# Optimization experiments

Hardware: AMD Instinct MI355X
Metric: run time of the kernel (lower is better)

## Reference

```python
import jax, jax.numpy as jnp
import numpy as np

B, S, H = 2, 2048, 2048
NH, NKV, HD = 16, 4, 128
THETA = 1000000.0

def _rope_tables(seq_len, dim, theta):
    inv_freq = 1.0 / (theta ** (np.arange(0, dim, 2, dtype=np.float32) / dim))
    t = np.arange(seq_len, dtype=np.float32)
    freqs = np.outer(t, inv_freq)                      # [S, dim/2]
    emb = np.concatenate([freqs, freqs], axis=-1)      # [S, dim]
    return jnp.asarray(np.cos(emb)), jnp.asarray(np.sin(emb))

def setup_inputs() -> dict:
    key = jax.random.key(0)
    ks = jax.random.split(key, 5)
    cos, sin = _rope_tables(S, HD, THETA)
    scale = 1.0 / np.sqrt(H)
    return {
        "x": jax.random.normal(ks[0], (B, S, H), jnp.float32),
        "cos": cos, "sin": sin,
        "wq": jax.random.normal(ks[1], (H, NH * HD), jnp.float32) * scale,
        "wk": jax.random.normal(ks[2], (H, NKV * HD), jnp.float32) * scale,
        "wv": jax.random.normal(ks[3], (H, NKV * HD), jnp.float32) * scale,
        "wo": jax.random.normal(ks[4], (NH * HD, H), jnp.float32) * scale,
    }

def _rotate_half(t):
    h = t.shape[-1] // 2
    return jnp.concatenate([-t[..., h:], t[..., :h]], axis=-1)

def reference(x, cos, sin, wq, wk, wv, wo):
    b, s, _ = x.shape
    n_rep = NH // NKV
    q = (x @ wq).reshape(b, s, NH, HD)    # [b,s,nh,hd]
    k = (x @ wk).reshape(b, s, NKV, HD)
    v = (x @ wv).reshape(b, s, NKV, HD)
    # RoPE: cos/sin [s,hd] broadcast over batch and heads
    c = cos[None, :, None, :]
    sn = sin[None, :, None, :]
    q = q * c + _rotate_half(q) * sn
    k = k * c + _rotate_half(k) * sn
    # GQA: repeat kv heads n_rep times
    k = jnp.repeat(k, n_rep, axis=2)      # [b,s,nh,hd]
    v = jnp.repeat(v, n_rep, axis=2)
    q = q.transpose(0, 2, 1, 3)           # [b,nh,s,hd]
    k = k.transpose(0, 2, 1, 3)
    v = v.transpose(0, 2, 1, 3)
    scores = jnp.einsum('bhqd,bhkd->bhqk', q, k) / jnp.sqrt(jnp.float32(HD))
    causal = jnp.tril(jnp.ones((s, s), dtype=bool))
    scores = jnp.where(causal[None, None], scores, jnp.float32(-jnp.inf))
    attn = jax.nn.softmax(scores.astype(jnp.float32), axis=-1).astype(q.dtype)
    out = jnp.einsum('bhqk,bhkd->bhqd', attn, v)
    out = out.transpose(0, 2, 1, 3).reshape(b, s, NH * HD)
    return out @ wo
```

## Files before the change

### kernel.cpp

```cpp
#include <hip/hip_runtime.h>
#include <hip/hip_bf16.h>

#define Bb 2
#define Ss 2048
#define Hh 2048
#define NH 16
#define NKV 4
#define HD 128
#define NREP (NH / NKV)
#define Mrows (Bb * Ss)
#define NQKV (NH*HD + 2*NKV*HD)

using short8 = __attribute__((ext_vector_type(8))) short;
using f32x4  = __attribute__((ext_vector_type(4))) float;

__device__ __forceinline__ unsigned short f2b(float f) {
  union { float f; unsigned u; } v; v.f = f;
  return (unsigned short)((v.u + 0x7fffu + ((v.u >> 16) & 1u)) >> 16);
}

__device__ __forceinline__ void gload16(const void* g, void* l) {
  __builtin_amdgcn_global_load_lds(
      (const __attribute__((address_space(1))) unsigned int*)g,
      (__attribute__((address_space(3))) unsigned int*)l, 16, 0, 0);
}

__global__ void prep(const float* __restrict__ x, unsigned short* __restrict__ xb,
                     const float* __restrict__ wq, const float* __restrict__ wk,
                     const float* __restrict__ wv, unsigned short* __restrict__ wqkvt,
                     const float* __restrict__ wo, unsigned short* __restrict__ wot) {
  __shared__ float tile[32][33];
  const int bid = blockIdx.x;
  const int t = threadIdx.x;
  if (bid < 8192) {
    int i = (bid * 256 + t) * 4;
    float4 f = *(const float4*)(x + i);
    ushort4 o;
    o.x = f2b(f.x); o.y = f2b(f.y); o.z = f2b(f.z); o.w = f2b(f.w);
    *(ushort4*)(xb + i) = o;
    return;
  }
  const int tx = t & 31, ty = t >> 5;
  if (bid < 8192 + 6144) {
    int idx = bid - 8192;
    int n0 = (idx % 96) * 32, k0 = (idx / 96) * 32;
    const float* src; int base, C;
    if (n0 < Hh)            { src = wq; base = 0;        C = NH * HD; }
    else if (n0 < Hh + 512) { src = wk; base = Hh;       C = NKV * HD; }
    else                    { src = wv; base = Hh + 512; C = NKV * HD; }
    int ng = n0 + tx;
    int cmg = ng;
    if (ng < Hh + 512) {
      int j = ng & 127;
      cmg = (ng & ~127) + ((j >> 5) << 4) + (j & 15) + ((j >> 4) & 1) * 64;
    }
    int col = cmg - base;
    #pragma unroll
    for (int i = ty; i < 32; i += 8)
      tile[i][tx] = src[(long)(k0 + i) * C + col];
    __syncthreads();
    #pragma unroll
    for (int i = ty; i < 32; i += 8)
      wqkvt[(long)(n0 + i) * Hh + k0 + tx] = f2b(tile[tx][i]);
  } else {
    int idx = bid - 8192 - 6144;
    int n0 = (idx % 64) * 32, k0 = (idx / 64) * 32;
    #pragma unroll
    for (int i = ty; i < 32; i += 8)
      tile[i][tx] = wo[(long)(k0 + i) * Hh + n0 + tx];
    __syncthreads();
    #pragma unroll
    for (int i = ty; i < 32; i += 8)
      wot[(long)(n0 + i) * Hh + k0 + tx] = f2b(tile[tx][i]);
  }
}

__global__ __launch_bounds__(512, 2) void gemm_qkv(const unsigned short* __restrict__ A,
                                                   const unsigned short* __restrict__ Bt,
                                                   const float* __restrict__ cosT,
                                                   const float* __restrict__ sinT,
                                                   unsigned short* __restrict__ qt,
                                                   unsigned short* __restrict__ kt,
                                                   unsigned short* __restrict__ vt) {
  __shared__ unsigned short As[2][256 * 64];
  __shared__ unsigned short Bs[2][256 * 64];
  const int t = threadIdx.x;
  const int lane = t & 63, wid = t >> 6;
  const int quad = lane >> 4, l16 = lane & 15;
  const int nt = blockIdx.x >> 4, mt = blockIdx.x & 15;
  const int n0 = nt * 256, m0 = mt * 256;
  const int wm = (wid >> 2) * 128, wn = (wid & 3) * 64;
  const bool isv = nt >= 10;
  const int Kk = Hh;

  const int sg = (lane & 7) ^ (lane >> 3);
  const int srow = wid * 8 + (lane >> 3);
  const unsigned short* Ag = A  + (long)(m0 + srow) * Kk + sg * 8;
  const unsigned short* Bg = Bt + (long)(n0 + srow) * Kk + sg * 8;

  f32x4 acc[8][4] = {};
  short8 aH[4][2], bH[2][2];

#define STAGE_A(buf, k0) { _Pragma("unroll") for (int i = 0; i < 4; i++) \
    gload16(Ag + (long)i * 64 * Kk + (k0), &As[buf][wid * 512 + i * 4096]); }
#define STAGE_B(buf, k0) { _Pragma("unroll") for (int i = 0; i < 4; i++) \
    gload16(Bg + (long)i * 64 * Kk + (k0), &Bs[buf][wid * 512 + i * 4096]); }
#define LDA(buf, mh) { _Pragma("unroll") for (int qq = 0; qq < 4; qq++) \
    _Pragma("unroll") for (int ks = 0; ks < 2; ks++) \
      aH[qq][ks] = *(const short8*)(&As[buf][(wm + (mh) * 64 + qq * 16 + l16) * 64 + \
                                             (((ks * 4 + quad) ^ (l16 & 7)) * 8)]); }
#define LDB(buf, nh) { _Pragma("unroll") for (int qq = 0; qq < 2; qq++) \
    _Pragma("unroll") for (int ks = 0; ks < 2; ks++) \
      bH[qq][ks] = *(const short8*)(&Bs[buf][(wn + (nh) * 32 + qq * 16 + l16) * 64 + \
                                             (((ks * 4 + quad) ^ (l16 & 7)) * 8)]); }
#define MM(mh, nh) { __builtin_amdgcn_s_setprio(1); \
    if (!isv) { \
      _Pragma("unroll") for (int qq = 0; qq < 4; qq++) \
      _Pragma("unroll") for (int n2 = 0; n2 < 2; n2++) \
      _Pragma("unroll") for (int ks = 0; ks < 2; ks++) \
        acc[(mh)*4+qq][(nh)*2+n2] = __builtin_amdgcn_mfma_f32_16x16x32_bf16( \
            aH[qq][ks], bH[n2][ks], acc[(mh)*4+qq][(nh)*2+n2], 0, 0, 0); \
    } else { \
      _Pragma("unroll") for (int qq = 0; qq < 4; qq++) \
      _Pragma("unroll") for (int n2 = 0; n2 < 2; n2++) \
      _Pragma("unroll") for (int ks = 0; ks < 2; ks++) \
        acc[(mh)*4+qq][(nh)*2+n2] = __builtin_amdgcn_mfma_f32_16x16x32_bf16( \
            bH[n2][ks], aH[qq][ks], acc[(mh)*4+qq][(nh)*2+n2], 0, 0, 0); \
    } __builtin_amdgcn_s_setprio(0); }
#define BAR() __builtin_amdgcn_s_barrier()
#define LGK0() asm volatile("s_waitcnt lgkmcnt(0)" ::: "memory")

  STAGE_A(0, 0); STAGE_B(0, 0);
  asm volatile("s_waitcnt vmcnt(0)" ::: "memory");
  BAR();

  for (int kt2 = 0; kt2 < Kk / 64; ++kt2) {
    const int cur = kt2 & 1, nxt = cur ^ 1;
    const long k0n = (long)(kt2 + 1) * 64;
    const bool pf = (kt2 + 1 < Kk / 64);
    LDA(cur, 0); LDB(cur, 0);
    if (pf) STAGE_A(nxt, k0n);
    BAR(); LGK0(); MM(0, 0); BAR();
    LDB(cur, 1);
    if (pf) STAGE_B(nxt, k0n);
    BAR(); LGK0(); MM(0, 1); BAR();
    LDA(cur, 1);
    BAR(); LGK0(); MM(1, 1); BAR();
    LDB(cur, 0);
    BAR(); LGK0(); MM(1, 0);
    asm volatile("s_waitcnt vmcnt(0)" ::: "memory");
    BAR();
  }

#undef STAGE_A
#undef STAGE_B
#undef LDA
#undef LDB
#undef MM
#undef BAR
#undef LGK0

  if (!isv) {
    #pragma unroll
    for (int MI = 0; MI < 8; MI++)
      #pragma unroll
      for (int r = 0; r < 4; r++) {
        int srw = m0 + wm + MI * 16 + quad * 4 + r;
        int bb = srw >> 11, s = srw & (Ss - 1);
        const float* cr = cosT + (long)s * HD;
        const float* sr = sinT + (long)s * HD;
        #pragma unroll
        for (int NI = 0; NI < 4; NI += 2) {
          int cb = n0 + wn + NI * 16;
          bool isq = cb < NH * HD;
          int hh = isq ? (cb >> 7) : ((cb - NH * HD) >> 7);
          unsigned short* dst = isq ? qt + (((long)bb * NH + hh) * Ss + s) * HD
                                    : kt + (((long)bb * NKV + hh) * Ss + s) * HD;
          int d = (((cb & 127) >> 5) << 4) + l16;
          float cc = cr[d], sn = sr[d];
          float x0 = acc[MI][NI][r], x1 = acc[MI][NI + 1][r];
          dst[d]      = f2b(x0 * cc - x1 * sn);
          dst[d + 64] = f2b(x1 * cc + x0 * sn);
        }
      }
  } else {
    #pragma unroll
    for (int MI = 0; MI < 8; MI++) {
      int srw = m0 + wm + MI * 16 + l16;
      int bb = srw >> 11, s = srw & (Ss - 1);
      #pragma unroll
      for (int NI = 0; NI < 4; NI++)
        #pragma unroll
        for (int r = 0; r < 4; r++) {
          int vcol = n0 - (NH * HD + NKV * HD) + wn + NI * 16 + quad * 4 + r;
          int kvh = vcol >> 7, d = vcol & 127;
          vt[(((long)bb * NKV + kvh) * HD + d) * Ss + s] = f2b(acc[MI][NI][r]);
        }
    }
  }
}

__global__ __launch_bounds__(256) void gemm_bt(const unsigned short* __restrict__ A,
                                               const unsigned short* __restrict__ Bt,
                                               float* __restrict__ Cv,
                                               int Mm, int Nn, int Kk) {
  __shared__ unsigned short As[128 * 64];
  __shared__ unsigned short Bs[128 * 64];
  const int t = threadIdx.x;
  const int lane = t & 63, wave = t >> 6;
  const int quad = lane >> 4, l16 = lane & 15;
  const int n0 = (blockIdx.x >> 5) * 128, m0 = (blockIdx.x & 31) * 128;
  const int wm = (wave >> 1) * 64, wn = (wave & 1) * 64;

  f32x4 acc[4][4] = {};

  const int srow = t >> 3;
  const int sgr  = (t & 7) ^ (srow & 7);
  const unsigned short* Ag = A  + (long)(m0 + srow) * Kk + sgr * 8;
  const unsigned short* Bg = Bt + (long)(n0 + srow) * Kk + sgr * 8;
  unsigned short* lA = As + (wave * 64) * 8;
  unsigned short* lB = Bs + (wave * 64) * 8;

  for (int k0 = 0; k0 < Kk; k0 += 64) {
    #pragma unroll
    for (int i = 0; i < 4; i++)
      gload16(Ag + (long)i * 32 * Kk + k0, lA + i * 256 * 8);
    #pragma unroll
    for (int i = 0; i < 4; i++)
      gload16(Bg + (long)i * 32 * Kk + k0, lB + i * 256 * 8);
    __syncthreads();

    #pragma unroll
    for (int sub = 0; sub < 2; sub++) {
      short8 af[4], bf[4];
      #pragma unroll
      for (int i = 0; i < 4; i++)
        af[i] = *(const short8*)(As + (wm + i * 16 + l16) * 64 + (((sub * 4 + quad) ^ (l16 & 7)) * 8));
      #pragma unroll
      for (int i = 0; i < 4; i++)
        bf[i] = *(const short8*)(Bs + (wn + i * 16 + l16) * 64 + (((sub * 4 + quad) ^ (l16 & 7)) * 8));

      #pragma unroll
      for (int mi = 0; mi < 4; mi++)
        #pragma unroll
        for (int ni = 0; ni < 4; ni++)
          acc[mi][ni] = __builtin_amdgcn_mfma_f32_16x16x32_bf16(af[mi], bf[ni], acc[mi][ni], 0, 0, 0);
    }
    __syncthreads();
  }

  #pragma unroll
  for (int mi = 0; mi < 4; mi++)
    #pragma unroll
    for (int ni = 0; ni < 4; ni++)
      #pragma unroll
      for (int r = 0; r < 4; r++) {
        long row = m0 + wm + mi * 16 + quad * 4 + r;
        long col = n0 + wn + ni * 16 + l16;
        Cv[row * Nn + col] = acc[mi][ni][r];
      }
}

__global__ __launch_bounds__(256, 2) void flash_attn(const unsigned short* __restrict__ qt,
                                                     const unsigned short* __restrict__ kt,
                                                     const unsigned short* __restrict__ vt,
                                                     unsigned short* __restrict__ out) {
  __shared__ unsigned short Ks[2][64 * 128];
  __shared__ unsigned short Vs[2][128 * 64];

  const int w = threadIdx.x >> 6, lane = threadIdx.x & 63;
  const int quad = lane >> 4, l16 = lane & 15;
  const int r8 = lane >> 3, c8 = lane & 7;
  const int idx = blockIdx.x;
  const int xcd = idx & 7;
  const int b = xcd >> 2, kvh = xcd & 3;
  const int rest = idx >> 3;
  const int k16 = rest >> 2;
  const int qblk = (k16 < 8) ? (15 - k16) : (k16 - 8);
  const int h = kvh * NREP + (rest & 3);
  const int q0w = qblk * 128 + w * 32;

  const unsigned short* Qb = qt + ((long)b * NH + h) * Ss * HD;
  const unsigned short* Kb = kt + ((long)b * NKV + kvh) * Ss * HD;
  const unsigned short* Vb = vt + ((long)b * NKV + kvh) * HD * Ss;
  const int nch = (qblk + 1) * 2;

  #pragma unroll
  for (int i = 0; i < 4; i++) {
    int rho = i * 16 + w * 4 + quad;
    int key = (rho & 32) + ((rho >> 2) & 3) * 8 + ((rho >> 4) & 1) * 4 + (rho & 3);
    int sg = l16 ^ (w * 4 + quad);
    gload16(Kb + (long)key * HD + sg * 8, &Ks[0][(i * 256 + w * 64) * 8]);
  }
  #pragma unroll
  for (int i = 0; i < 4; i++) {
    int dv = i * 32 + w * 8 + r8;
    int sg = c8 ^ r8;
    gload16(Vb + (long)dv * Ss + sg * 8, &Vs[0][(i * 256 + w * 64) * 8]);
  }

  short8 qf[2][4];
  #pragma unroll
  for (int qi = 0; qi < 2; qi++)
    #pragma unroll
    for (int kc = 0; kc < 4; kc++)
      qf[qi][kc] = *(const short8*)(Qb + (long)(q0w + qi * 16 + l16) * HD + kc * 32 + quad * 8);

  f32x4 accO[2][8] = {};
  float l_i[2];
  l_i[0] = l_i[1] = 0.f;
  const float cscale = 1.4426950408889634f * 0.08838834764831845f;

  for (int c = 0; c < nch; ++c) {
    const unsigned short* Ksb = Ks[c & 1];
    const unsigned short* Vsb = Vs[c & 1];

    if (c + 1 < nch) {
      const int k0 = (c + 1) * 64;
      unsigned short* Kd = Ks[(c + 1) & 1];
      unsigned short* Vd = Vs[(c + 1) & 1];
      #pragma unroll
      for (int i = 0; i < 4; i++) {
        int rho = i * 16 + w * 4 + quad;
        int key = (rho & 32) + ((rho >> 2) & 3) * 8 + ((rho >> 4) & 1) * 4 + (rho & 3);
        int sg = l16 ^ (w * 4 + quad);
        gload16(Kb + (long)(k0 + key) * HD + sg * 8, Kd + (i * 256 + w * 64) * 8);
      }
      #pragma unroll
      for (int i = 0; i < 4; i++) {
        int dv = i * 32 + w * 8 + r8;
        int sg = c8 ^ r8;
        gload16(Vb + (long)dv * Ss + k0 + sg * 8, Vd + (i * 256 + w * 64) * 8);
      }
      asm volatile("s_waitcnt vmcnt(8)" ::: "memory");
    } else {
      asm volatile("s_waitcnt vmcnt(0)" ::: "memory");
    }
    asm volatile("s_barrier" ::: "memory");

    if (c * 64 < q0w + 32) {
      f32x4 sc[2][4] = {};
      #pragma unroll
      for (int T = 0; T < 4; T++)
        #pragma unroll
        for (int kc = 0; kc < 4; kc++) {
          short8 kf = *(const short8*)(Ksb + ((16 * T + l16) * 16 + ((kc * 4 + quad) ^ l16)) * 8);
          #pragma unroll
          for (int qi = 0; qi < 2; qi++)
            sc[qi][T] = __builtin_amdgcn_mfma_f32_16x16x32_bf16(kf, qf[qi][kc], sc[qi][T], 0, 0, 0);
        }

      if ((c + 1) * 64 - 1 > q0w) {
        #pragma unroll
        for (int qi = 0; qi < 2; qi++) {
          int qq = q0w + qi * 16 + l16;
          #pragma unroll
          for (int T = 0; T < 4; T++)
            #pragma unroll
            for (int r = 0; r < 4; r++) {
              int ka = c * 64 + (T >> 1) * 32 + quad * 8 + (T & 1) * 4 + r;
              if (ka > qq) sc[qi][T][r] = -__builtin_inff();
            }
        }
      }

      short8 pf[2][2];
      #pragma unroll
      for (int qi = 0; qi < 2; qi++) {
        float p[4][4], rs = 0.f;
        #pragma unroll
        for (int T = 0; T < 4; T++)
          #pragma unroll
          for (int r = 0; r < 4; r++) {
            p[T][r] = __builtin_amdgcn_exp2f(sc[qi][T][r] * cscale);
            rs += p[T][r];
          }
        rs += __shfl_xor(rs, 16);
        rs += __shfl_xor(rs, 32);
        l_i[qi] += rs;

        #pragma unroll
        for (int c2 = 0; c2 < 2; c2++) {
          short8 f;
          f[0] = (short)f2b(p[2 * c2][0]);     f[1] = (short)f2b(p[2 * c2][1]);
          f[2] = (short)f2b(p[2 * c2][2]);     f[3] = (short)f2b(p[2 * c2][3]);
          f[4] = (short)f2b(p[2 * c2 + 1][0]); f[5] = (short)f2b(p[2 * c2 + 1][1]);
          f[6] = (short)f2b(p[2 * c2 + 1][2]); f[7] = (short)f2b(p[2 * c2 + 1][3]);
          pf[qi][c2] = f;
        }
      }

      #pragma unroll
      for (int c2 = 0; c2 < 2; c2++)
        #pragma unroll
        for (int Dt = 0; Dt < 8; Dt++) {
          short8 vf = *(const short8*)(Vsb + ((16 * Dt + l16) * 8 + ((4 * c2 + quad) ^ (l16 & 7))) * 8);
          #pragma unroll
          for (int qi = 0; qi < 2; qi++)
            accO[qi][Dt] = __builtin_amdgcn_mfma_f32_16x16x32_bf16(vf, pf[qi][c2], accO[qi][Dt], 0, 0, 0);
        }
    }

    asm volatile("s_waitcnt lgkmcnt(0)" ::: "memory");
    asm volatile("s_barrier" ::: "memory");
  }

  #pragma unroll
  for (int qi = 0; qi < 2; qi++) {
    float inv = 1.f / l_i[qi];
    long orow = (long)b * Ss + q0w + qi * 16 + l16;
    #pragma unroll
    for (int Dt = 0; Dt < 8; Dt++) {
      ushort4 o;
      o.x = f2b(accO[qi][Dt][0] * inv);
      o.y = f2b(accO[qi][Dt][1] * inv);
      o.z = f2b(accO[qi][Dt][2] * inv);
      o.w = f2b(accO[qi][Dt][3] * inv);
      *(ushort4*)(out + orow * (NH * HD) + h * HD + Dt * 16 + quad * 4) = o;
    }
  }
}

extern "C" void kernel_launch(void* const* d_in, const int* in_sizes, int n_in,
                              void* d_out, int out_size, void* d_ws, size_t ws_size,
                              hipStream_t stream) {
  const float* x    = (const float*)d_in[0];
  const float* cosT = (const float*)d_in[1];
  const float* sinT = (const float*)d_in[2];
  const float* wq   = (const float*)d_in[3];
  const float* wk   = (const float*)d_in[4];
  const float* wv   = (const float*)d_in[5];
  const float* wo   = (const float*)d_in[6];
  float* out = (float*)d_out;

  char* ws = (char*)d_ws;
  unsigned short* xb    = (unsigned short*)(ws);
  unsigned short* wqkvt = (unsigned short*)(ws + (16l << 20));
  unsigned short* wot   = (unsigned short*)(ws + (28l << 20));
  unsigned short* qt    = (unsigned short*)(ws + (36l << 20));
  unsigned short* kt    = (unsigned short*)(ws + (52l << 20));
  unsigned short* vt    = (unsigned short*)(ws + (56l << 20));
  unsigned short* attno = xb;

  prep<<<8192 + 6144 + 4096, 256, 0, stream>>>(x, xb, wq, wk, wv, wqkvt, wo, wot);

  gemm_qkv<<<(NQKV / 256) * (Mrows / 256), 512, 0, stream>>>(xb, wqkvt, cosT, sinT, qt, kt, vt);

  flash_attn<<<(Ss / 128) * NH * Bb, 256, 0, stream>>>(qt, kt, vt, attno);

  gemm_bt<<<(Hh / 128) * (Mrows / 128), 256, 0, stream>>>(attno, wot, out, Mrows, Hh, Hh);
}
```

Before: 309.3 us.

## Simplify QKV GEMM main loop to one barrier per k-tile, drop setprio

The fine-grained four-phase schedule in the QKV projection GEMM is replaced. That schedule had a barrier and an lgkmcnt wait around every MFMA group, s_setprio raises, and an explicit vmcnt wait. Now the next tile's global-to-LDS loads are issued up front, all four LDS-read/MFMA groups run back to back, and a single __syncthreads ends each k-tile. The aim is to cut barrier overhead and let the compiler interleave LDS reads with MFMAs. The trade-off is the lost wave-priority ping-pong overlap between waves. Correctness also now depends on __syncthreads waiting for the async LDS loads.

```diff
diff --git a/kernel.cpp b/kernel.cpp
--- a/kernel.cpp
+++ b/kernel.cpp
@@ -113,7 +113,7 @@
     _Pragma("unroll") for (int ks = 0; ks < 2; ks++) \
       bH[qq][ks] = *(const short8*)(&Bs[buf][(wn + (nh) * 32 + qq * 16 + l16) * 64 + \
                                              (((ks * 4 + quad) ^ (l16 & 7)) * 8)]); }
-#define MM(mh, nh) { __builtin_amdgcn_s_setprio(1); \
+#define MM(mh, nh) { \
     if (!isv) { \
       _Pragma("unroll") for (int qq = 0; qq < 4; qq++) \
       _Pragma("unroll") for (int n2 = 0; n2 < 2; n2++) \
@@ -126,30 +126,23 @@
       _Pragma("unroll") for (int ks = 0; ks < 2; ks++) \
         acc[(mh)*4+qq][(nh)*2+n2] = __builtin_amdgcn_mfma_f32_16x16x32_bf16( \
             bH[n2][ks], aH[qq][ks], acc[(mh)*4+qq][(nh)*2+n2], 0, 0, 0); \
-    } __builtin_amdgcn_s_setprio(0); }
-#define BAR() __builtin_amdgcn_s_barrier()
-#define LGK0() asm volatile("s_waitcnt lgkmcnt(0)" ::: "memory")
+    } }
 
   STAGE_A(0, 0); STAGE_B(0, 0);
-  asm volatile("s_waitcnt vmcnt(0)" ::: "memory");
-  BAR();
+  __syncthreads();
 
   for (int kt2 = 0; kt2 < Kk / 64; ++kt2) {
     const int cur = kt2 & 1, nxt = cur ^ 1;
-    const long k0n = (long)(kt2 + 1) * 64;
-    const bool pf = (kt2 + 1 < Kk / 64);
-    LDA(cur, 0); LDB(cur, 0);
-    if (pf) STAGE_A(nxt, k0n);
-    BAR(); LGK0(); MM(0, 0); BAR();
-    LDB(cur, 1);
-    if (pf) STAGE_B(nxt, k0n);
-    BAR(); LGK0(); MM(0, 1); BAR();
-    LDA(cur, 1);
-    BAR(); LGK0(); MM(1, 1); BAR();
-    LDB(cur, 0);
-    BAR(); LGK0(); MM(1, 0);
-    asm volatile("s_waitcnt vmcnt(0)" ::: "memory");
-    BAR();
+    if (kt2 + 1 < Kk / 64) {
+      const long k0n = (long)(kt2 + 1) * 64;
+      STAGE_A(nxt, k0n);
+      STAGE_B(nxt, k0n);
+    }
+    LDA(cur, 0); LDB(cur, 0); MM(0, 0);
+    LDB(cur, 1);              MM(0, 1);
+    LDA(cur, 1);              MM(1, 1);
+    LDB(cur, 0);              MM(1, 0);
+    __syncthreads();
   }
 
 #undef STAGE_A
@@ -157,8 +150,6 @@
 #undef LDA
 #undef LDB
 #undef MM
-#undef BAR
-#undef LGK0
 
   if (!isv) {
     #pragma unroll
```

After: 324.6 us. 1.05x slower.
